# Performance work log

Hardware: AMD Instinct MI355X
Metric: run time of the kernel (lower is better)

Reference implementation:

```python
import jax, jax.numpy as jnp
import numpy as np

NUM_HEADS = 16
D_MODEL = 1024
HEAD_DIM = D_MODEL // NUM_HEADS  # 64
BATCH = 2
SEQ = 2048
ROPE_THETA = 10000.0


def apply_rope(x, positions):
    # x: (B, S, H, hd), positions: (B, S) int
    hd = x.shape[-1]
    half = hd // 2
    inv_freq = 1.0 / (ROPE_THETA ** (jnp.arange(half, dtype=jnp.float32) / half))  # (half,)
    angles = positions[..., None].astype(jnp.float32) * inv_freq                   # (B, S, half)
    cos = jnp.cos(angles)[..., None, :]  # (B, S, 1, half) broadcast over heads
    sin = jnp.sin(angles)[..., None, :]
    x1, x2 = x[..., :half], x[..., half:]
    return jnp.concatenate([x1 * cos - x2 * sin, x1 * sin + x2 * cos], axis=-1).astype(x.dtype)


def setup_inputs() -> dict:
    key = jax.random.key(0)
    k1, k2, k3 = jax.random.split(key, 3)
    inputs = jax.random.normal(k1, (BATCH, SEQ, D_MODEL), dtype=jnp.float32)
    # Linear weights stored as (in, out); pytorch y = x @ W.T, equivalent math.
    w_in = jax.random.normal(k2, (D_MODEL, 3 * D_MODEL), dtype=jnp.float32) * (D_MODEL ** -0.5)
    w_out = jax.random.normal(k3, (D_MODEL, D_MODEL), dtype=jnp.float32) * (D_MODEL ** -0.5)
    positions = jnp.tile(jnp.arange(SEQ, dtype=jnp.int64)[None, :], (BATCH, 1))
    return {"inputs": inputs, "positions": positions, "w_in": w_in, "w_out": w_out}


def reference(inputs, positions, w_in, w_out):
    B, S, _ = inputs.shape
    # fused QKV projection; per-head layout is (heads, 3*head_dim) -> chunk into q,k,v
    proj = inputs @ w_in                                   # (B, S, 3*D)
    proj = proj.reshape(B, S, NUM_HEADS, 3 * HEAD_DIM)     # (B, S, H, 3*hd)
    q, k, v = jnp.split(proj, 3, axis=-1)                  # each (B, S, H, hd)
    q = apply_rope(q, positions)
    k = apply_rope(k, positions)
    # flex_attention with block_mask=None: full softmax attention, scale 1/sqrt(hd)
    scale = 1.0 / np.sqrt(HEAD_DIM)
    scores = jnp.einsum('bqhd,bkhd->bhqk', q, k) * scale   # (B, H, S, S)
    attn = jax.nn.softmax(scores, axis=-1)
    out = jnp.einsum('bhqk,bkhd->bqhd', attn, v)           # (B, S, H, hd)
    out = out.reshape(B, S, NUM_HEADS * HEAD_DIM)
    return out @ w_out                                     # (B, S, D)
```

## Files before the change

### kernel.cpp

```cpp
#include <hip/hip_runtime.h>

typedef float f32x4 __attribute__((ext_vector_type(4)));
typedef short s16x8 __attribute__((ext_vector_type(8)));
typedef unsigned short u16;

#define SQ 2048
#define DM 1024
#define NH 16
#define HD 64

__device__ __forceinline__ u16 f2bf(float f) {
    union { float f; unsigned u; } v; v.f = f;
    unsigned u = v.u + 0x7FFFu + ((v.u >> 16) & 1u);
    return (u16)(u >> 16);
}

__device__ __forceinline__ f32x4 mfma_bf16(s16x8 a, s16x8 b, f32x4 c) {
    asm("v_mfma_f32_16x16x32_bf16 %0, %1, %2, %0" : "+v"(c) : "v"(a), "v"(b));
    return c;
}

__device__ __forceinline__ void gload16(const void* g, const void* lds_base) {
    __builtin_amdgcn_global_load_lds(
        (const __attribute__((address_space(1))) unsigned int*)g,
        (__attribute__((address_space(3))) unsigned int*)lds_base,
        16, 0, 0);
}

__global__ void k_convert(const float* __restrict__ in, u16* __restrict__ out, int n4) {
    int i = blockIdx.x * blockDim.x + threadIdx.x;
    int stride = gridDim.x * blockDim.x;
    for (; i < n4; i += stride) {
        float4 f = ((const float4*)in)[i];
        ushort4 o;
        o.x = f2bf(f.x); o.y = f2bf(f.y); o.z = f2bf(f.z); o.w = f2bf(f.w);
        ((ushort4*)out)[i] = o;
    }
}

__global__ void k_transpose_bf16(const float* __restrict__ in, u16* __restrict__ out, int R, int C) {
    __shared__ float tile[32][33];
    int c0 = blockIdx.x * 32, r0 = blockIdx.y * 32;
    int tx = threadIdx.x, ty = threadIdx.y;
#pragma unroll
    for (int i = 0; i < 32; i += 8)
        tile[ty + i][tx] = in[(size_t)(r0 + ty + i) * C + c0 + tx];
    __syncthreads();
#pragma unroll
    for (int i = 0; i < 32; i += 8)
        out[(size_t)(c0 + ty + i) * R + r0 + tx] = f2bf(tile[tx][ty + i]);
}

__global__ void k_transpose_v(const u16* __restrict__ in, u16* __restrict__ out) {
    __shared__ u16 tile[32][33];
    int bh = blockIdx.z;
    int c0 = blockIdx.x * 32;
    int r0 = blockIdx.y * 32;
    const u16* src = in + (size_t)bh * SQ * HD;
    u16* dst = out + (size_t)bh * HD * SQ;
    int tx = threadIdx.x, ty = threadIdx.y;
#pragma unroll
    for (int i = 0; i < 32; i += 8)
        tile[ty + i][tx] = src[(size_t)(r0 + ty + i) * HD + c0 + tx];
    __syncthreads();
#pragma unroll
    for (int i = 0; i < 32; i += 8)
        dst[(size_t)(c0 + ty + i) * SQ + r0 + tx] = tile[tx][ty + i];
}

__global__ __launch_bounds__(256) void k_gemm_bt(
    const u16* __restrict__ A, const u16* __restrict__ Bt, float* __restrict__ C,
    int M, int N, int K)
{
    __shared__ u16 As[128 * 64];
    __shared__ u16 Bs[128 * 64];
    const int tid = threadIdx.x;
    const int lane = tid & 63;
    const int wave = tid >> 6;
    const int wr = wave >> 1, wc = wave & 1;
    const int m0 = blockIdx.y * 128, n0 = blockIdx.x * 128;
    const int l16 = lane & 15, g4 = lane >> 4;

    const int srow = lane >> 3;
    const int scol = (lane & 7) ^ srow;

    f32x4 acc[4][4] = {};

    for (int k0 = 0; k0 < K; k0 += 64) {
        __syncthreads();
#pragma unroll
        for (int j = 0; j < 4; ++j) {
            int rt = (wave * 4 + j) * 8 + srow;
            gload16(&A[(size_t)(m0 + rt) * K + k0 + scol * 8], &As[(wave * 4 + j) * 512]);
            gload16(&Bt[(size_t)(n0 + rt) * K + k0 + scol * 8], &Bs[(wave * 4 + j) * 512]);
        }
        __syncthreads();
#pragma unroll
        for (int kc = 0; kc < 2; ++kc) {
            s16x8 af[4], bfr[4];
#pragma unroll
            for (int i = 0; i < 4; ++i) {
                int ra = wr * 64 + i * 16 + l16;
                int offa = (kc * 64 + g4 * 16) ^ ((ra & 7) << 4);
                af[i] = *(const s16x8*)((const char*)As + ra * 128 + offa);
                int rb = wc * 64 + i * 16 + l16;
                int offb = (kc * 64 + g4 * 16) ^ ((rb & 7) << 4);
                bfr[i] = *(const s16x8*)((const char*)Bs + rb * 128 + offb);
            }
#pragma unroll
            for (int mi = 0; mi < 4; ++mi)
#pragma unroll
                for (int ni = 0; ni < 4; ++ni)
                    acc[mi][ni] = mfma_bf16(af[mi], bfr[ni], acc[mi][ni]);
        }
    }
    asm volatile("s_nop 7\ns_nop 7");
#pragma unroll
    for (int mi = 0; mi < 4; ++mi)
#pragma unroll
        for (int ni = 0; ni < 4; ++ni)
#pragma unroll
            for (int r = 0; r < 4; ++r) {
                int row = m0 + wr * 64 + mi * 16 + g4 * 4 + r;
                int col = n0 + wc * 64 + ni * 16 + l16;
                C[(size_t)row * N + col] = acc[mi][ni][r];
            }
}

__global__ __launch_bounds__(512) void k_rope_pack(
    const float* __restrict__ proj, const int* __restrict__ positions,
    u16* __restrict__ Q, u16* __restrict__ Kd, u16* __restrict__ V)
{
    int bs = blockIdx.x;
    int h = threadIdx.x >> 5;
    int j = threadIdx.x & 31;
    const float* p = proj + (size_t)bs * 3072 + h * 192;
    float q1 = p[j],       q2 = p[j + 32];
    float k1 = p[64 + j],  k2 = p[96 + j];
    float v1 = p[128 + j], v2 = p[160 + j];
    int pos = positions[bs];
    float inv = __expf(-(float)j * (9.210340371976184f / 32.0f));
    float ang = (float)pos * inv;
    float sn, cs;
    sincosf(ang, &sn, &cs);
    int b = bs >> 11, s = bs & (SQ - 1);
    size_t o = ((size_t)(b * NH + h) * SQ + s) * HD + j;
    Q[o]      = f2bf(0.125f * (q1 * cs - q2 * sn));
    Q[o + 32] = f2bf(0.125f * (q1 * sn + q2 * cs));
    Kd[o]      = f2bf(k1 * cs - k2 * sn);
    Kd[o + 32] = f2bf(k1 * sn + k2 * cs);
    V[o]      = f2bf(v1);
    V[o + 32] = f2bf(v2);
}

__global__ __launch_bounds__(256) void k_attn(
    const u16* __restrict__ Q, const u16* __restrict__ Kg, const u16* __restrict__ Vt,
    u16* __restrict__ O)
{
    __shared__ alignas(16) u16 Ks[64 * 64];
    __shared__ alignas(16) u16 Vs[64 * 64];
    __shared__ alignas(16) u16 Ps[4 * 16 * 72];
    const int tid = threadIdx.x, lane = tid & 63, wave = tid >> 6;
    const int bid = blockIdx.x;
    const int vb = (bid & 7) * 128 + (bid >> 3);
    const int bh = vb >> 5;
    const int q0 = (vb & 31) * 64;
    const int l16 = lane & 15, g4 = lane >> 4;
    const size_t base  = (size_t)bh * SQ * HD;
    const size_t vbase = (size_t)bh * HD * SQ;

    s16x8 qf[2];
    {
        const u16* qrow = Q + base + (size_t)(q0 + wave * 16 + l16) * HD + g4 * 8;
        qf[0] = *(const s16x8*)(qrow);
        qf[1] = *(const s16x8*)(qrow + 32);
    }
    f32x4 oacc[4] = {};
    f32x4 lsum = {0.f, 0.f, 0.f, 0.f};

    u16* Pw = Ps + wave * 16 * 72;
    const int r8 = lane >> 3, c8 = lane & 7;
    const int sw = c8 ^ r8;

    for (int t = 0; t < SQ / 64; ++t) {
        const int kk0 = t * 64;
        __syncthreads();
#pragma unroll
        for (int j = 0; j < 2; ++j) {
            int row = wave * 16 + j * 8 + r8;
            gload16(&Kg[base + (size_t)(kk0 + row) * HD + sw * 8],
                    &Ks[(wave * 16 + j * 8) * 64]);
            gload16(&Vt[vbase + (size_t)row * SQ + kk0 + sw * 8],
                    &Vs[(wave * 16 + j * 8) * 64]);
        }
        __syncthreads();

        f32x4 sacc[4] = {};
        __builtin_amdgcn_s_setprio(1);
#pragma unroll
        for (int kc = 0; kc < 2; ++kc)
#pragma unroll
            for (int ni = 0; ni < 4; ++ni) {
                int row = ni * 16 + l16;
                const char* p = (const char*)Ks + row * 128 +
                                ((kc * 64 + g4 * 16) ^ ((l16 & 7) << 4));
                sacc[ni] = mfma_bf16(qf[kc], *(const s16x8*)p, sacc[ni]);
            }
        __builtin_amdgcn_s_setprio(0);
        asm volatile("s_nop 7\ns_nop 7");

#pragma unroll
        for (int ni = 0; ni < 4; ++ni)
#pragma unroll
            for (int r = 0; r < 4; ++r) {
                float pv = __expf(sacc[ni][r]);
                lsum[r] += pv;
                Pw[(g4 * 4 + r) * 72 + ni * 16 + l16] = f2bf(pv);
            }

        __builtin_amdgcn_s_setprio(1);
#pragma unroll
        for (int kc = 0; kc < 2; ++kc) {
            s16x8 af = *(const s16x8*)(&Pw[l16 * 72 + kc * 32 + g4 * 8]);
#pragma unroll
            for (int di = 0; di < 4; ++di) {
                int row = di * 16 + l16;
                const char* p = (const char*)Vs + row * 128 +
                                ((kc * 64 + g4 * 16) ^ ((l16 & 7) << 4));
                oacc[di] = mfma_bf16(af, *(const s16x8*)p, oacc[di]);
            }
        }
        __builtin_amdgcn_s_setprio(0);
    }
    asm volatile("s_nop 7\ns_nop 7");

#pragma unroll
    for (int off = 1; off < 16; off <<= 1)
#pragma unroll
        for (int r = 0; r < 4; ++r) lsum[r] += __shfl_xor(lsum[r], off, 16);

    const int b = bh >> 4, h = bh & (NH - 1);
#pragma unroll
    for (int r = 0; r < 4; ++r) {
        float inv = 1.0f / lsum[r];
#pragma unroll
        for (int di = 0; di < 4; ++di) {
            int qrow = q0 + wave * 16 + g4 * 4 + r;
            O[((size_t)(b * SQ + qrow)) * DM + h * HD + di * 16 + l16] =
                f2bf(oacc[di][r] * inv);
        }
    }
}

extern "C" void kernel_launch(void* const* d_in, const int* in_sizes, int n_in,
                              void* d_out, int out_size, void* d_ws, size_t ws_size,
                              hipStream_t stream)
{
    const float* inputs    = (const float*)d_in[0];
    const int*   positions = (const int*)d_in[1];
    const float* w_in      = (const float*)d_in[2];
    const float* w_out     = (const float*)d_in[3];
    float* out = (float*)d_out;

    char* w = (char*)d_ws;
    float* proj  = (float*)(w);
    u16* Vtb     = (u16*)(w);
    u16* inb     = (u16*)(w + 50331648);
    u16* winT    = (u16*)(w + 58720256);
    u16* woutT   = (u16*)(w + 65011712);
    u16* Qb      = (u16*)(w + 67108864);
    u16* Kb      = (u16*)(w + 75497472);
    u16* Vb      = (u16*)(w + 83886080);
    u16* attnb   = (u16*)(w + 92274688);

    k_convert<<<2048, 256, 0, stream>>>(inputs, inb, (4096 * 1024) / 4);
    k_transpose_bf16<<<dim3(96, 32), dim3(32, 8), 0, stream>>>(w_in, winT, 1024, 3072);
    k_transpose_bf16<<<dim3(32, 32), dim3(32, 8), 0, stream>>>(w_out, woutT, 1024, 1024);
    k_gemm_bt<<<dim3(24, 32), 256, 0, stream>>>(inb, winT, proj, 4096, 3072, 1024);
    k_rope_pack<<<4096, 512, 0, stream>>>(proj, positions, Qb, Kb, Vb);
    k_transpose_v<<<dim3(2, 64, 32), dim3(32, 8), 0, stream>>>(Vb, Vtb);
    k_attn<<<1024, 256, 0, stream>>>(Qb, Kb, Vtb, attnb);
    k_gemm_bt<<<dim3(8, 32), 256, 0, stream>>>(attnb, woutT, out, 4096, 1024, 1024);
}
```

Before: 146.7 us.

## Fuse RoPE and Q/K/V packing into the QKV projection GEMM epilogue

Replaces the separate fp32 projection write plus the rope/pack kernel with a GEMM whose epilogue applies RoPE, scales Q, and writes bf16 Q/K/V in head-major layout directly. This removes the round trip of a 48MB fp32 intermediate through memory and one kernel launch. The epilogue uses partner accumulators (ni^2) inside the same 64-column tile for the rotation pair, and per-element exp/sincos with uncoalesced 2-byte scattered stores, which may cost some epilogue efficiency. It uses the faster lower-accuracy __sincosf for angles up to about 2047 rad.

New measurement: 140.1 us. 4.5% less time.

```diff
diff --git a/kernel.cpp b/kernel.cpp
--- a/kernel.cpp
+++ b/kernel.cpp
@@ -8,6 +8,7 @@
 #define DM 1024
 #define NH 16
 #define HD 64
+
 
 __device__ __forceinline__ u16 f2bf(float f) {
     union { float f; unsigned u; } v; v.f = f;
@@ -127,30 +128,90 @@
             }
 }
 
-__global__ __launch_bounds__(512) void k_rope_pack(
-    const float* __restrict__ proj, const int* __restrict__ positions,
-    u16* __restrict__ Q, u16* __restrict__ Kd, u16* __restrict__ V)
+__global__ __launch_bounds__(256) void k_gemm1_rope(
+    const u16* __restrict__ A, const u16* __restrict__ Bt,
+    const int* __restrict__ positions,
+    u16* __restrict__ Qb, u16* __restrict__ Kb, u16* __restrict__ Vb)
 {
-    int bs = blockIdx.x;
-    int h = threadIdx.x >> 5;
-    int j = threadIdx.x & 31;
-    const float* p = proj + (size_t)bs * 3072 + h * 192;
-    float q1 = p[j],       q2 = p[j + 32];
-    float k1 = p[64 + j],  k2 = p[96 + j];
-    float v1 = p[128 + j], v2 = p[160 + j];
-    int pos = positions[bs];
-    float inv = __expf(-(float)j * (9.210340371976184f / 32.0f));
-    float ang = (float)pos * inv;
-    float sn, cs;
-    sincosf(ang, &sn, &cs);
-    int b = bs >> 11, s = bs & (SQ - 1);
-    size_t o = ((size_t)(b * NH + h) * SQ + s) * HD + j;
-    Q[o]      = f2bf(0.125f * (q1 * cs - q2 * sn));
-    Q[o + 32] = f2bf(0.125f * (q1 * sn + q2 * cs));
-    Kd[o]      = f2bf(k1 * cs - k2 * sn);
-    Kd[o + 32] = f2bf(k1 * sn + k2 * cs);
-    V[o]      = f2bf(v1);
-    V[o + 32] = f2bf(v2);
+    const int M = 4096, N = 3072, K = 1024;
+    __shared__ u16 As[128 * 64];
+    __shared__ u16 Bs[128 * 64];
+    const int tid = threadIdx.x;
+    const int lane = tid & 63;
+    const int wave = tid >> 6;
+    const int wr = wave >> 1, wc = wave & 1;
+    const int m0 = blockIdx.y * 128, n0 = blockIdx.x * 128;
+    const int l16 = lane & 15, g4 = lane >> 4;
+
+    const int srow = lane >> 3;
+    const int scol = (lane & 7) ^ srow;
+
+    f32x4 acc[4][4] = {};
+
+    for (int k0 = 0; k0 < K; k0 += 64) {
+        __syncthreads();
+#pragma unroll
+        for (int j = 0; j < 4; ++j) {
+            int rt = (wave * 4 + j) * 8 + srow;
+            gload16(&A[(size_t)(m0 + rt) * K + k0 + scol * 8], &As[(wave * 4 + j) * 512]);
+            gload16(&Bt[(size_t)(n0 + rt) * K + k0 + scol * 8], &Bs[(wave * 4 + j) * 512]);
+        }
+        __syncthreads();
+#pragma unroll
+        for (int kc = 0; kc < 2; ++kc) {
+            s16x8 af[4], bfr[4];
+#pragma unroll
+            for (int i = 0; i < 4; ++i) {
+                int ra = wr * 64 + i * 16 + l16;
+                int offa = (kc * 64 + g4 * 16) ^ ((ra & 7) << 4);
+                af[i] = *(const s16x8*)((const char*)As + ra * 128 + offa);
+                int rb = wc * 64 + i * 16 + l16;
+                int offb = (kc * 64 + g4 * 16) ^ ((rb & 7) << 4);
+                bfr[i] = *(const s16x8*)((const char*)Bs + rb * 128 + offb);
+            }
+#pragma unroll
+            for (int mi = 0; mi < 4; ++mi)
+#pragma unroll
+                for (int ni = 0; ni < 4; ++ni)
+                    acc[mi][ni] = mfma_bf16(af[mi], bfr[ni], acc[mi][ni]);
+        }
+    }
+    asm volatile("s_nop 7\ns_nop 7");
+
+#pragma unroll
+    for (int mi = 0; mi < 4; ++mi)
+#pragma unroll
+        for (int r = 0; r < 4; ++r) {
+            int row = m0 + wr * 64 + mi * 16 + g4 * 4 + r;
+            int pos = positions[row];
+            int b = row >> 11, s = row & (SQ - 1);
+            float fpos = (float)pos;
+#pragma unroll
+            for (int ni = 0; ni < 4; ++ni) {
+                float v = acc[mi][ni][r];
+                int col = n0 + wc * 64 + ni * 16 + l16;
+                int h = col / 192;
+                int c = col - h * 192;
+                int kind = c >> 6;
+                int cc = c & 63;
+                size_t o = (((size_t)(b * NH + h) * SQ + s)) * HD + cc;
+                if (kind == 2) {
+                    Vb[o] = f2bf(v);
+                } else {
+                    float partner = acc[mi][ni ^ 2][r];
+                    int j = cc & 31;
+                    int hi = cc >> 5;
+                    float inv = __expf(-(float)j * (9.210340371976184f / 32.0f));
+                    float sn, cs;
+                    __sincosf(fpos * inv, &sn, &cs);
+                    float x1 = hi ? partner : v;
+                    float x2 = hi ? v : partner;
+                    float outv = hi ? (x1 * sn + x2 * cs) : (x1 * cs - x2 * sn);
+                    if (kind == 0) outv *= 0.125f;
+                    (kind == 0 ? Qb : Kb)[o] = f2bf(outv);
+                }
+            }
+        }
 }
 
 __global__ __launch_bounds__(256) void k_attn(
@@ -263,7 +324,6 @@
     float* out = (float*)d_out;
 
     char* w = (char*)d_ws;
-    float* proj  = (float*)(w);
     u16* Vtb     = (u16*)(w);
     u16* inb     = (u16*)(w + 50331648);
     u16* winT    = (u16*)(w + 58720256);
@@ -276,8 +336,7 @@
     k_convert<<<2048, 256, 0, stream>>>(inputs, inb, (4096 * 1024) / 4);
     k_transpose_bf16<<<dim3(96, 32), dim3(32, 8), 0, stream>>>(w_in, winT, 1024, 3072);
     k_transpose_bf16<<<dim3(32, 32), dim3(32, 8), 0, stream>>>(w_out, woutT, 1024, 1024);
-    k_gemm_bt<<<dim3(24, 32), 256, 0, stream>>>(inb, winT, proj, 4096, 3072, 1024);
-    k_rope_pack<<<4096, 512, 0, stream>>>(proj, positions, Qb, Kb, Vb);
+    k_gemm1_rope<<<dim3(24, 32), 256, 0, stream>>>(inb, winT, positions, Qb, Kb, Vb);
     k_transpose_v<<<dim3(2, 64, 32), dim3(32, 8), 0, stream>>>(Vb, Vtb);
     k_attn<<<1024, 256, 0, stream>>>(Qb, Kb, Vtb, attnb);
     k_gemm_bt<<<dim3(8, 32), 256, 0, stream>>>(attnb, woutT, out, 4096, 1024, 1024);
```
